# Optimization experiments

Hardware: AMD Instinct MI355X
Metric: run time of the kernel (lower is better)

## Reference

```python
import jax, jax.numpy as jnp
import numpy as np

N = 100000   # nodes
E = 600000   # edges
F_IN = 128
F_OUT = 128


def setup_inputs() -> dict:
    key = jax.random.key(0)
    k1, k2, k3, k4 = jax.random.split(key, 4)
    x = jax.random.normal(k1, (N, F_IN), dtype=jnp.float32)
    edge_index = jax.random.randint(k2, (2, E), 0, N, dtype=jnp.int32)
    edge_wt = jnp.ones((E,), dtype=jnp.float32)  # learnable param, init ones
    # GCNConv weight (glorot-ish scale) and bias
    weight = jax.random.normal(k3, (F_IN, F_OUT), dtype=jnp.float32) / np.sqrt(F_IN).astype(np.float32)
    bias = jnp.zeros((F_OUT,), dtype=jnp.float32)
    u = jax.random.normal(k4, (F_IN,), dtype=jnp.float32)  # spectral-norm power-iter buffer
    return {"x": x, "edge_index": edge_index, "edge_wt": edge_wt,
            "weight": weight, "bias": bias, "u": u}


def _l2norm(v):
    return v / (jnp.linalg.norm(v) + 1e-12)


def reference(x, edge_index, edge_wt, weight, bias, u):
    # --- spectral norm on GCNConv weight (one power iteration, torch semantics:
    # u, v are stop-gradiented buffers; sigma = u^T W v keeps grad wrt W) ---
    W_sg = jax.lax.stop_gradient(weight)
    v = _l2norm(W_sg.T @ jax.lax.stop_gradient(u))
    u1 = _l2norm(W_sg @ v)
    sigma = u1 @ (weight @ v)
    W_sn = weight / sigma

    # --- per-edge sigmoid-weighted GCNConv with self loops + symmetric norm ---
    w = jax.nn.sigmoid(edge_wt)                      # [E]
    row, col = edge_index[0], edge_index[1]
    loop = jnp.arange(N, dtype=edge_index.dtype)
    row_a = jnp.concatenate([row, loop])             # [E+N]
    col_a = jnp.concatenate([col, loop])
    w_a = jnp.concatenate([w, jnp.ones((N,), w.dtype)])  # self-loop weight 1

    deg = jax.ops.segment_sum(w_a, col_a, num_segments=N)   # [N]
    dinv = jnp.where(deg > 0, deg ** -0.5, 0.0)
    norm = dinv[row_a] * w_a * dinv[col_a]           # [E+N]

    xw = x @ W_sn                                    # [N, F_OUT]
    msgs = norm[:, None] * xw[row_a]                 # [E+N, F_OUT] gather
    out = jax.ops.segment_sum(msgs, col_a, num_segments=N) + bias  # scatter
    return out
```

## Files before the change

kernel.cpp:

```cpp
#include <hip/hip_runtime.h>
#include <math.h>

#define F 128

typedef __bf16 bf16_t;
typedef unsigned long long u64;
typedef __attribute__((ext_vector_type(8))) bf16_t bf16x8;
typedef __attribute__((ext_vector_type(4))) bf16_t bf16x4;
typedef __attribute__((ext_vector_type(4))) float floatx4;

#define DEG_SCALE 32768.0f
#define DEG_INV   (1.0f / 32768.0f)

__global__ __launch_bounds__(256) void init_spec_k(const float* __restrict__ W,
                                                   const float* __restrict__ u,
                                                   bf16_t* __restrict__ Wt,
                                                   unsigned* __restrict__ dc, int n) {
    if (blockIdx.x == 0) {
        __shared__ float Wl[F][F + 1];
        __shared__ float ul[F];
        __shared__ float sv[F];
        __shared__ float red[4];
        __shared__ float snorm, s_is;
        int t = threadIdx.x;
        if (t < F) ul[t] = u[t];
        for (int i = t; i < F * 32; i += 256) {
            int r = i >> 5, c4 = (i & 31) * 4;
            float4 v = *(const float4*)(W + r * F + c4);
            Wl[r][c4] = v.x; Wl[r][c4 + 1] = v.y; Wl[r][c4 + 2] = v.z; Wl[r][c4 + 3] = v.w;
        }
        __syncthreads();
        float s = 0.f;
        if (t < F)
            for (int i = 0; i < F; ++i) s += Wl[i][t] * ul[i];
        float ss = (t < F) ? s * s : 0.f;
        for (int o = 32; o > 0; o >>= 1) ss += __shfl_down(ss, o);
        if ((t & 63) == 0) red[t >> 6] = ss;
        __syncthreads();
        if (t == 0) snorm = sqrtf(red[0] + red[1] + red[2] + red[3]);
        __syncthreads();
        if (t < F) sv[t] = s / (snorm + 1e-12f);
        __syncthreads();
        float s2 = 0.f;
        if (t < F)
            for (int j = 0; j < F; ++j) s2 += Wl[t][j] * sv[j];
        float ss2 = (t < F) ? s2 * s2 : 0.f;
        for (int o = 32; o > 0; o >>= 1) ss2 += __shfl_down(ss2, o);
        if ((t & 63) == 0) red[t >> 6] = ss2;
        __syncthreads();
        if (t == 0) {
            float a = red[0] + red[1] + red[2] + red[3];
            float nt = sqrtf(a);
            float sigma = a / (nt + 1e-12f);
            s_is = 1.0f / sigma;
        }
        __syncthreads();
        float is = s_is;
        for (int i = t; i < F * 16; i += 256) {
            int nrow = i >> 4, c = (i & 15) * 8;
            bf16x8 v;
#pragma unroll
            for (int j = 0; j < 8; ++j) v[j] = (bf16_t)(Wl[c + j][nrow] * is);
            *(bf16x8*)(Wt + nrow * F + c) = v;
        }
    } else {
        int i = (blockIdx.x - 1) * 256 + threadIdx.x;
        if (i < n) dc[i] = 0u;
    }
}

__global__ __launch_bounds__(256) void count_k(const int* __restrict__ col,
                                               const float* __restrict__ wt,
                                               unsigned* __restrict__ dc,
                                               int* __restrict__ rank, int e_cnt) {
    int e4 = (blockIdx.x * 256 + threadIdx.x) * 4;
    if (e4 + 3 < e_cnt) {
        int4 c = *(const int4*)(col + e4);
        float4 w = *(const float4*)(wt + e4);
        unsigned p0 = (1u << 24) | (unsigned)rintf(DEG_SCALE / (1.0f + expf(-w.x)));
        unsigned p1 = (1u << 24) | (unsigned)rintf(DEG_SCALE / (1.0f + expf(-w.y)));
        unsigned p2 = (1u << 24) | (unsigned)rintf(DEG_SCALE / (1.0f + expf(-w.z)));
        unsigned p3 = (1u << 24) | (unsigned)rintf(DEG_SCALE / (1.0f + expf(-w.w)));
        unsigned o0 = atomicAdd(dc + c.x, p0);
        unsigned o1 = atomicAdd(dc + c.y, p1);
        unsigned o2 = atomicAdd(dc + c.z, p2);
        unsigned o3 = atomicAdd(dc + c.w, p3);
        *(int4*)(rank + e4) = make_int4((int)(o0 >> 24), (int)(o1 >> 24),
                                        (int)(o2 >> 24), (int)(o3 >> 24));
    } else {
        for (int e = e4; e < e_cnt; ++e) {
            int c = col[e];
            unsigned pkt = (1u << 24) | (unsigned)rintf(DEG_SCALE / (1.0f + expf(-wt[e])));
            unsigned old = atomicAdd(dc + c, pkt);
            rank[e] = (int)(old >> 24);
        }
    }
}

#define GBM 64
#define LDK 136
__global__ __launch_bounds__(256) void gemm_k(const float* __restrict__ x,
                                              const bf16_t* __restrict__ Wt,
                                              bf16_t* __restrict__ xwh, int nrows) {
    __shared__ bf16_t As[GBM * LDK];
    int tid = threadIdx.x;
    int rowBase = blockIdx.x * GBM;

    for (int i = tid; i < GBM * 32; i += 256) {
        int r = i >> 5, c4 = (i & 31) * 4;
        float4 xv = make_float4(0.f, 0.f, 0.f, 0.f);
        if (rowBase + r < nrows) xv = *(const float4*)(x + (size_t)(rowBase + r) * F + c4);
        bf16x4 v;
        v.x = (bf16_t)xv.x; v.y = (bf16_t)xv.y; v.z = (bf16_t)xv.z; v.w = (bf16_t)xv.w;
        *(bf16x4*)(As + r * LDK + c4) = v;
    }
    __syncthreads();

    int wave = tid >> 6, lane = tid & 63;
    int l16 = lane & 15, q = lane >> 4;
    int mrow = wave * 16;

    floatx4 acc[8];
#pragma unroll
    for (int nt = 0; nt < 8; ++nt) acc[nt] = (floatx4){0.f, 0.f, 0.f, 0.f};

#pragma unroll
    for (int kt = 0; kt < 4; ++kt) {
        bf16x8 a = *(bf16x8*)(As + (mrow + l16) * LDK + kt * 32 + q * 8);
#pragma unroll
        for (int nt = 0; nt < 8; ++nt) {
            bf16x8 bb = *(const bf16x8*)(Wt + (size_t)(nt * 16 + l16) * F + kt * 32 + q * 8);
            acc[nt] = __builtin_amdgcn_mfma_f32_16x16x32_bf16(a, bb, acc[nt], 0, 0, 0);
        }
    }
    __syncthreads();

#pragma unroll
    for (int nt = 0; nt < 8; ++nt) {
#pragma unroll
        for (int r = 0; r < 4; ++r)
            As[(mrow + q * 4 + r) * LDK + nt * 16 + l16] = (bf16_t)acc[nt][r];
    }
    __syncthreads();

    for (int i = tid; i < GBM * 16; i += 256) {
        int r = i >> 4, c = (i & 15) * 8;
        if (rowBase + r < nrows)
            *(bf16x8*)(xwh + (size_t)(rowBase + r) * F + c) = *(bf16x8*)(As + r * LDK + c);
    }
}

#define STILE 1024
__global__ __launch_bounds__(256) void scan1_k(const unsigned* __restrict__ dc,
                                               int* __restrict__ bsum,
                                               float* __restrict__ dinv, int n) {
    __shared__ int red[256];
    int t = threadIdx.x;
    int base = blockIdx.x * STILE + t * 4;
    int s = 0;
    for (int i = 0; i < 4; ++i) {
        if (base + i < n) {
            unsigned v = dc[base + i];
            s += (int)(v >> 24);
            float d = 1.0f + (float)(v & 0xFFFFFFu) * DEG_INV;
            dinv[base + i] = 1.0f / sqrtf(d);
        }
    }
    red[t] = s;
    __syncthreads();
    for (int o = 128; o > 0; o >>= 1) { if (t < o) red[t] += red[t + o]; __syncthreads(); }
    if (t == 0) bsum[blockIdx.x] = red[0];
}

__global__ __launch_bounds__(256) void scan3_k(const unsigned* __restrict__ dc,
                                               const int* __restrict__ bsum,
                                               int* __restrict__ offsets, int g, int n) {
    __shared__ int sc[256];
    int t = threadIdx.x;
    int bid = blockIdx.x;
    int bbase = 0;
    for (int i = 0; i < bid; ++i) bbase += bsum[i];
    int base = bid * STILE + t * 4;
    int v[4] = {0, 0, 0, 0};
    for (int i = 0; i < 4; ++i)
        if (base + i < n) v[i] = (int)(dc[base + i] >> 24);
    int ts = v[0] + v[1] + v[2] + v[3];
    sc[t] = ts;
    __syncthreads();
    for (int o = 1; o < 256; o <<= 1) {
        int val = sc[t];
        int add = (t >= o) ? sc[t - o] : 0;
        __syncthreads();
        sc[t] = val + add;
        __syncthreads();
    }
    int run = bbase + sc[t] - ts;
    for (int i = 0; i < 4; ++i) {
        if (base + i < n) offsets[base + i] = run;
        run += v[i];
    }
    if (bid == g - 1 && t == 255) offsets[n] = bbase + sc[255];
}

__global__ __launch_bounds__(256) void fill_k(const int* __restrict__ row,
                                              const int* __restrict__ col,
                                              const float* __restrict__ wt,
                                              const float* __restrict__ dinv,
                                              const int* __restrict__ offsets,
                                              const int* __restrict__ rank,
                                              int2* __restrict__ edat, int e_cnt) {
    int e = blockIdx.x * 256 + threadIdx.x;
    if (e < e_cnt) {
        int r = row[e], c = col[e];
        float w = 1.0f / (1.0f + expf(-wt[e]));
        float nv = dinv[r] * w * dinv[c];
        int p = offsets[c] + rank[e];
        edat[p] = make_int2(r, __float_as_int(nv));
    }
}

template <int MODE>
__global__ __launch_bounds__(256) void gather_t(const int* __restrict__ offsets,
                                                const int2* __restrict__ edat,
                                                const float* __restrict__ dinv,
                                                const float* __restrict__ x,
                                                const bf16_t* __restrict__ xh,
                                                const float* __restrict__ bias,
                                                float* __restrict__ out, int n) {
    int node = blockIdx.x * 4 + (threadIdx.x >> 6);
    if (node >= n) return;
    int lane = threadIdx.x & 63;
    const float2* x2 = (const float2*)x;
    float dv = dinv[node];
    float2 acc;
    if (MODE) {
        unsigned vs = ((const unsigned*)(xh + (size_t)node * F))[lane];
        acc.x = dv * dv * __uint_as_float(vs << 16);
        acc.y = dv * dv * __uint_as_float(vs & 0xFFFF0000u);
    } else {
        float2 xv = x2[(size_t)node * 64 + lane];
        acc.x = dv * dv * xv.x;
        acc.y = dv * dv * xv.y;
    }
    int s = offsets[node], e = offsets[node + 1];
    for (int b = s; b < e; b += 64) {
        int cnt = min(64, e - b);
        int2 ed = make_int2(0, 0);
        if (lane < cnt) ed = edat[b + lane];
        int j = 0;
        for (; j + 4 <= cnt; j += 4) {
            int r0 = __shfl(ed.x, j + 0), r1 = __shfl(ed.x, j + 1);
            int r2 = __shfl(ed.x, j + 2), r3 = __shfl(ed.x, j + 3);
            float n0 = __int_as_float(__shfl(ed.y, j + 0));
            float n1 = __int_as_float(__shfl(ed.y, j + 1));
            float n2 = __int_as_float(__shfl(ed.y, j + 2));
            float n3 = __int_as_float(__shfl(ed.y, j + 3));
            if (MODE) {
                unsigned v0 = ((const unsigned*)(xh + (size_t)r0 * F))[lane];
                unsigned v1 = ((const unsigned*)(xh + (size_t)r1 * F))[lane];
                unsigned v2 = ((const unsigned*)(xh + (size_t)r2 * F))[lane];
                unsigned v3 = ((const unsigned*)(xh + (size_t)r3 * F))[lane];
                acc.x = fmaf(n0, __uint_as_float(v0 << 16), acc.x);
                acc.y = fmaf(n0, __uint_as_float(v0 & 0xFFFF0000u), acc.y);
                acc.x = fmaf(n1, __uint_as_float(v1 << 16), acc.x);
                acc.y = fmaf(n1, __uint_as_float(v1 & 0xFFFF0000u), acc.y);
                acc.x = fmaf(n2, __uint_as_float(v2 << 16), acc.x);
                acc.y = fmaf(n2, __uint_as_float(v2 & 0xFFFF0000u), acc.y);
                acc.x = fmaf(n3, __uint_as_float(v3 << 16), acc.x);
                acc.y = fmaf(n3, __uint_as_float(v3 & 0xFFFF0000u), acc.y);
            } else {
                float2 a0 = x2[(size_t)r0 * 64 + lane];
                float2 a1 = x2[(size_t)r1 * 64 + lane];
                float2 a2 = x2[(size_t)r2 * 64 + lane];
                float2 a3 = x2[(size_t)r3 * 64 + lane];
                acc.x = fmaf(n0, a0.x, acc.x); acc.y = fmaf(n0, a0.y, acc.y);
                acc.x = fmaf(n1, a1.x, acc.x); acc.y = fmaf(n1, a1.y, acc.y);
                acc.x = fmaf(n2, a2.x, acc.x); acc.y = fmaf(n2, a2.y, acc.y);
                acc.x = fmaf(n3, a3.x, acc.x); acc.y = fmaf(n3, a3.y, acc.y);
            }
        }
        for (; j < cnt; ++j) {
            int r = __shfl(ed.x, j);
            float nv = __int_as_float(__shfl(ed.y, j));
            if (MODE) {
                unsigned v = ((const unsigned*)(xh + (size_t)r * F))[lane];
                acc.x = fmaf(nv, __uint_as_float(v << 16), acc.x);
                acc.y = fmaf(nv, __uint_as_float(v & 0xFFFF0000u), acc.y);
            } else {
                float2 xr = x2[(size_t)r * 64 + lane];
                acc.x = fmaf(nv, xr.x, acc.x);
                acc.y = fmaf(nv, xr.y, acc.y);
            }
        }
    }
    if (MODE) {
        float2 bv = ((const float2*)bias)[lane];
        acc.x += bv.x;
        acc.y += bv.y;
    }
    ((float2*)out)[(size_t)node * 64 + lane] = acc;
}

__global__ __launch_bounds__(256) void gemm_mfma_k(float* __restrict__ io,
                                                   const bf16_t* __restrict__ Wt,
                                                   const float* __restrict__ bias,
                                                   int nrows) {
    __shared__ bf16_t As[GBM * LDK];
    int tid = threadIdx.x;
    int rowBase = blockIdx.x * GBM;

    for (int i = tid; i < GBM * 32; i += 256) {
        int r = i >> 5, c4 = (i & 31) * 4;
        float4 xv = make_float4(0.f, 0.f, 0.f, 0.f);
        if (rowBase + r < nrows) xv = *(const float4*)(io + (size_t)(rowBase + r) * F + c4);
        bf16x4 v;
        v.x = (bf16_t)xv.x; v.y = (bf16_t)xv.y; v.z = (bf16_t)xv.z; v.w = (bf16_t)xv.w;
        *(bf16x4*)(As + r * LDK + c4) = v;
    }
    __syncthreads();

    int wave = tid >> 6, lane = tid & 63;
    int l16 = lane & 15, q = lane >> 4;
    int mrow = wave * 16;

    floatx4 acc[8];
#pragma unroll
    for (int nt = 0; nt < 8; ++nt) acc[nt] = (floatx4){0.f, 0.f, 0.f, 0.f};

#pragma unroll
    for (int kt = 0; kt < 4; ++kt) {
        bf16x8 a = *(bf16x8*)(As + (mrow + l16) * LDK + kt * 32 + q * 8);
#pragma unroll
        for (int nt = 0; nt < 8; ++nt) {
            bf16x8 b = *(const bf16x8*)(Wt + (size_t)(nt * 16 + l16) * F + kt * 32 + q * 8);
            acc[nt] = __builtin_amdgcn_mfma_f32_16x16x32_bf16(a, b, acc[nt], 0, 0, 0);
        }
    }

#pragma unroll
    for (int nt = 0; nt < 8; ++nt) {
        int col = nt * 16 + l16;
        float bv = bias[col];
#pragma unroll
        for (int r = 0; r < 4; ++r) {
            int grow = rowBase + mrow + q * 4 + r;
            if (grow < nrows) io[(size_t)grow * F + col] = acc[nt][r] + bv;
        }
    }
}

extern "C" void kernel_launch(void* const* d_in, const int* in_sizes, int n_in,
                              void* d_out, int out_size, void* d_ws, size_t ws_size,
                              hipStream_t stream) {
    const float* x    = (const float*)d_in[0];
    const int*   ei   = (const int*)d_in[1];
    const float* ewt  = (const float*)d_in[2];
    const float* W    = (const float*)d_in[3];
    const float* bias = (const float*)d_in[4];
    const float* u    = (const float*)d_in[5];
    float* out = (float*)d_out;

    int n_nodes = in_sizes[0] / F;
    int e_cnt   = in_sizes[2];
    const int* row = ei;
    const int* col = ei + e_cnt;

    char* wsb = (char*)d_ws;
    float*    dinv    = (float*)wsb;
    size_t off = ((size_t)n_nodes * 4 + 15) & ~(size_t)15;
    unsigned* dc      = (unsigned*)(wsb + off);
    off += (size_t)n_nodes * 4;
    off = (off + 15) & ~(size_t)15;
    int*      offsets = (int*)(wsb + off);
    off += (size_t)(n_nodes + 1) * 4;
    off = (off + 15) & ~(size_t)15;
    int*      bsum    = (int*)(wsb + off);
    off += 2048 * 4;
    off = (off + 15) & ~(size_t)15;
    int*      rank    = (int*)(wsb + off);
    off += (size_t)e_cnt * 4;
    off = (off + 15) & ~(size_t)15;
    int2*     edat    = (int2*)(wsb + off);
    off += (size_t)e_cnt * 8;
    off = (off + 15) & ~(size_t)15;
    bf16_t*   Wt      = (bf16_t*)(wsb + off);
    off += (size_t)F * F * 2;
    bf16_t*   xwh     = (bf16_t*)(wsb + off);
    size_t need_bf16 = off + (size_t)n_nodes * F * 2;
    int use_bf16 = (ws_size >= need_bf16);

    int g_scan  = (n_nodes + STILE - 1) / STILE;
    int gCount  = (e_cnt + 1023) / 1024;
    int gInit   = (n_nodes + 255) / 256;
    int gGemm   = (n_nodes + GBM - 1) / GBM;

    init_spec_k<<<gInit + 1, 256, 0, stream>>>(W, u, Wt, dc, n_nodes);
    count_k<<<gCount, 256, 0, stream>>>(col, ewt, dc, rank, e_cnt);
    if (use_bf16)
        gemm_k<<<gGemm, 256, 0, stream>>>(x, Wt, xwh, n_nodes);
    scan1_k<<<g_scan, 256, 0, stream>>>(dc, bsum, dinv, n_nodes);
    scan3_k<<<g_scan, 256, 0, stream>>>(dc, bsum, offsets, g_scan, n_nodes);
    fill_k<<<(e_cnt + 255) / 256, 256, 0, stream>>>(row, col, ewt, dinv, offsets, rank,
                                                    edat, e_cnt);
    if (use_bf16) {
        gather_t<1><<<(n_nodes + 3) / 4, 256, 0, stream>>>(offsets, edat, dinv, x, xwh, bias,
                                                           out, n_nodes);
    } else {
        gather_t<0><<<(n_nodes + 3) / 4, 256, 0, stream>>>(offsets, edat, dinv, x, xwh, bias,
                                                           out, n_nodes);
        gemm_mfma_k<<<gGemm, 256, 0, stream>>>(out, Wt, bias, n_nodes);
    }
}
```

Measured before the change: 243.5 us.

## Fuse degree-count and GEMM into one launch with register-loaded A tiles

Merges the edge degree-count kernel and the bf16 GEMM kernel into a single launch, where the first blocks do the GEMM and the rest do the atomic counting, so the two independent phases overlap and one launch is saved. The GEMM also now loads its A fragments straight from global into registers instead of staging through shared memory, and each wave writes its output through a private shared tile without block-wide barriers. The risk is that the A-fragment global loads are less coalesced (strided per lane), and that the shared per-wave output buffers raise LDS use on the counting blocks too.

Result: faster. 218.3 us (-10.4%).

```diff
diff --git a/kernel.cpp b/kernel.cpp
--- a/kernel.cpp
+++ b/kernel.cpp
@@ -69,56 +69,64 @@
     }
 }
 
-__global__ __launch_bounds__(256) void count_k(const int* __restrict__ col,
-                                               const float* __restrict__ wt,
-                                               unsigned* __restrict__ dc,
-                                               int* __restrict__ rank, int e_cnt) {
-    int e4 = (blockIdx.x * 256 + threadIdx.x) * 4;
-    if (e4 + 3 < e_cnt) {
-        int4 c = *(const int4*)(col + e4);
-        float4 w = *(const float4*)(wt + e4);
-        unsigned p0 = (1u << 24) | (unsigned)rintf(DEG_SCALE / (1.0f + expf(-w.x)));
-        unsigned p1 = (1u << 24) | (unsigned)rintf(DEG_SCALE / (1.0f + expf(-w.y)));
-        unsigned p2 = (1u << 24) | (unsigned)rintf(DEG_SCALE / (1.0f + expf(-w.z)));
-        unsigned p3 = (1u << 24) | (unsigned)rintf(DEG_SCALE / (1.0f + expf(-w.w)));
-        unsigned o0 = atomicAdd(dc + c.x, p0);
-        unsigned o1 = atomicAdd(dc + c.y, p1);
-        unsigned o2 = atomicAdd(dc + c.z, p2);
-        unsigned o3 = atomicAdd(dc + c.w, p3);
-        *(int4*)(rank + e4) = make_int4((int)(o0 >> 24), (int)(o1 >> 24),
-                                        (int)(o2 >> 24), (int)(o3 >> 24));
-    } else {
-        for (int e = e4; e < e_cnt; ++e) {
-            int c = col[e];
-            unsigned pkt = (1u << 24) | (unsigned)rintf(DEG_SCALE / (1.0f + expf(-wt[e])));
-            unsigned old = atomicAdd(dc + c, pkt);
-            rank[e] = (int)(old >> 24);
-        }
-    }
-}
-
 #define GBM 64
 #define LDK 136
-__global__ __launch_bounds__(256) void gemm_k(const float* __restrict__ x,
-                                              const bf16_t* __restrict__ Wt,
-                                              bf16_t* __restrict__ xwh, int nrows) {
-    __shared__ bf16_t As[GBM * LDK];
+__global__ __launch_bounds__(256) void count_gemm_k(const int* __restrict__ col,
+                                                    const float* __restrict__ wt,
+                                                    unsigned* __restrict__ dc,
+                                                    int* __restrict__ rank, int e_cnt,
+                                                    const float* __restrict__ x,
+                                                    const bf16_t* __restrict__ Wt,
+                                                    bf16_t* __restrict__ xwh, int nrows,
+                                                    int gGemm) {
+    __shared__ bf16_t Os[4][16 * LDK];
+    int b = blockIdx.x;
+    if (b >= gGemm) {
+        int e4 = ((b - gGemm) * 256 + threadIdx.x) * 4;
+        if (e4 + 3 < e_cnt) {
+            int4 c = *(const int4*)(col + e4);
+            float4 w = *(const float4*)(wt + e4);
+            unsigned p0 = (1u << 24) | (unsigned)rintf(DEG_SCALE / (1.0f + expf(-w.x)));
+            unsigned p1 = (1u << 24) | (unsigned)rintf(DEG_SCALE / (1.0f + expf(-w.y)));
+            unsigned p2 = (1u << 24) | (unsigned)rintf(DEG_SCALE / (1.0f + expf(-w.z)));
+            unsigned p3 = (1u << 24) | (unsigned)rintf(DEG_SCALE / (1.0f + expf(-w.w)));
+            unsigned o0 = atomicAdd(dc + c.x, p0);
+            unsigned o1 = atomicAdd(dc + c.y, p1);
+            unsigned o2 = atomicAdd(dc + c.z, p2);
+            unsigned o3 = atomicAdd(dc + c.w, p3);
+            *(int4*)(rank + e4) = make_int4((int)(o0 >> 24), (int)(o1 >> 24),
+                                            (int)(o2 >> 24), (int)(o3 >> 24));
+        } else {
+            for (int e = e4; e < e_cnt; ++e) {
+                int c = col[e];
+                unsigned pkt = (1u << 24) | (unsigned)rintf(DEG_SCALE / (1.0f + expf(-wt[e])));
+                unsigned old = atomicAdd(dc + c, pkt);
+                rank[e] = (int)(old >> 24);
+            }
+        }
+        return;
+    }
     int tid = threadIdx.x;
-    int rowBase = blockIdx.x * GBM;
-
-    for (int i = tid; i < GBM * 32; i += 256) {
-        int r = i >> 5, c4 = (i & 31) * 4;
-        float4 xv = make_float4(0.f, 0.f, 0.f, 0.f);
-        if (rowBase + r < nrows) xv = *(const float4*)(x + (size_t)(rowBase + r) * F + c4);
-        bf16x4 v;
-        v.x = (bf16_t)xv.x; v.y = (bf16_t)xv.y; v.z = (bf16_t)xv.z; v.w = (bf16_t)xv.w;
-        *(bf16x4*)(As + r * LDK + c4) = v;
-    }
-    __syncthreads();
-
     int wave = tid >> 6, lane = tid & 63;
     int l16 = lane & 15, q = lane >> 4;
-    int mrow = wave * 16;
+    int wRow = b * GBM + wave * 16;
+
+    int arow = wRow + l16;
+    bool rok = (arow < nrows);
+    const float* xrow = x + (size_t)(rok ? arow : 0) * F;
+    bf16x8 a[4];
+#pragma unroll
+    for (int kt = 0; kt < 4; ++kt) {
+        float4 a0 = make_float4(0.f, 0.f, 0.f, 0.f), a1 = a0;
+        if (rok) {
+            a0 = *(const float4*)(xrow + kt * 32 + q * 8);
+            a1 = *(const float4*)(xrow + kt * 32 + q * 8 + 4);
+        }
+        bf16x8 v;
+        v[0] = (bf16_t)a0.x; v[1] = (bf16_t)a0.y; v[2] = (bf16_t)a0.z; v[3] = (bf16_t)a0.w;
+        v[4] = (bf16_t)a1.x; v[5] = (bf16_t)a1.y; v[6] = (bf16_t)a1.z; v[7] = (bf16_t)a1.w;
+        a[kt] = v;
+    }
 
     floatx4 acc[8];
 #pragma unroll
@@ -126,27 +134,27 @@
 
 #pragma unroll
     for (int kt = 0; kt < 4; ++kt) {
-        bf16x8 a = *(bf16x8*)(As + (mrow + l16) * LDK + kt * 32 + q * 8);
 #pragma unroll
         for (int nt = 0; nt < 8; ++nt) {
             bf16x8 bb = *(const bf16x8*)(Wt + (size_t)(nt * 16 + l16) * F + kt * 32 + q * 8);
-            acc[nt] = __builtin_amdgcn_mfma_f32_16x16x32_bf16(a, bb, acc[nt], 0, 0, 0);
-        }
-    }
-    __syncthreads();
-
+            acc[nt] = __builtin_amdgcn_mfma_f32_16x16x32_bf16(a[kt], bb, acc[nt], 0, 0, 0);
+        }
+    }
+
+    bf16_t* myOs = Os[wave];
 #pragma unroll
     for (int nt = 0; nt < 8; ++nt) {
 #pragma unroll
         for (int r = 0; r < 4; ++r)
-            As[(mrow + q * 4 + r) * LDK + nt * 16 + l16] = (bf16_t)acc[nt][r];
-    }
-    __syncthreads();
-
-    for (int i = tid; i < GBM * 16; i += 256) {
-        int r = i >> 4, c = (i & 15) * 8;
-        if (rowBase + r < nrows)
-            *(bf16x8*)(xwh + (size_t)(rowBase + r) * F + c) = *(bf16x8*)(As + r * LDK + c);
+            myOs[(q * 4 + r) * LDK + nt * 16 + l16] = (bf16_t)acc[nt][r];
+    }
+#pragma unroll
+    for (int j = 0; j < 4; ++j) {
+        int idx = j * 64 + lane;
+        int r = idx >> 4, c8 = (idx & 15) * 8;
+        int grow = wRow + r;
+        if (grow < nrows)
+            *(bf16x8*)(xwh + (size_t)grow * F + c8) = *(bf16x8*)(myOs + r * LDK + c8);
     }
 }
 
@@ -395,9 +403,13 @@
     int gGemm   = (n_nodes + GBM - 1) / GBM;
 
     init_spec_k<<<gInit + 1, 256, 0, stream>>>(W, u, Wt, dc, n_nodes);
-    count_k<<<gCount, 256, 0, stream>>>(col, ewt, dc, rank, e_cnt);
-    if (use_bf16)
-        gemm_k<<<gGemm, 256, 0, stream>>>(x, Wt, xwh, n_nodes);
+    if (use_bf16) {
+        count_gemm_k<<<gGemm + gCount, 256, 0, stream>>>(col, ewt, dc, rank, e_cnt, x, Wt,
+                                                         xwh, n_nodes, gGemm);
+    } else {
+        count_gemm_k<<<gCount, 256, 0, stream>>>(col, ewt, dc, rank, e_cnt, x, Wt,
+                                                 xwh, n_nodes, 0);
+    }
     scan1_k<<<g_scan, 256, 0, stream>>>(dc, bsum, dinv, n_nodes);
     scan3_k<<<g_scan, 256, 0, stream>>>(dc, bsum, offsets, g_scan, n_nodes);
     fill_k<<<(e_cnt + 255) / 256, 256, 0, stream>>>(row, col, ewt, dinv, offsets, rank,
```
